# Performance work log

Hardware: AMD Instinct MI355X
Metric: run time of the kernel (lower is better)

Reference implementation:

```python
import jax, jax.numpy as jnp
import numpy as np

N = 50000      # nodes
E = 600000     # edges (avg degree 12)
D = 128        # in_dim == hidden_dim
H = 4          # heads
HD = 32        # per-head dim (hidden_dim // heads)
NEG = 0.2      # GATv2 leaky_relu negative slope (PyG default)
EPS = 1e-5     # LayerNorm eps


def setup_inputs() -> dict:
    key = jax.random.key(0)
    ks = jax.random.split(key, 4)
    inp = {
        "x": jax.random.normal(ks[0], (N, D), jnp.float32),
        "edge_index": jax.random.randint(ks[1], (2, E), 0, N, dtype=jnp.int32),
    }
    glorot = 1.0 / np.sqrt(D)
    for i in range(2):
        k = jax.random.split(jax.random.fold_in(ks[2], i), 8)
        inp[f"Wl{i}"] = jax.random.normal(k[0], (D, H * HD), jnp.float32) * glorot
        inp[f"bl{i}"] = jnp.zeros((H * HD,), jnp.float32)
        inp[f"Wr{i}"] = jax.random.normal(k[1], (D, H * HD), jnp.float32) * glorot
        inp[f"br{i}"] = jnp.zeros((H * HD,), jnp.float32)
        inp[f"att{i}"] = jax.random.normal(k[2], (H, HD), jnp.float32) * (1.0 / np.sqrt(HD))
        inp[f"bias{i}"] = jnp.zeros((H * HD,), jnp.float32)
        inp[f"g{i}"] = jnp.ones((H * HD,), jnp.float32)   # LayerNorm gamma
        inp[f"b{i}"] = jnp.zeros((H * HD,), jnp.float32)  # LayerNorm beta
    return inp


def _gat_layer(h, src, dst, Wl, bl, Wr, br, att, bias, g, b):
    # GATv2: x_l from source nodes, x_r from destination nodes
    xl = (h @ Wl + bl).reshape(N, H, HD)
    xr = (h @ Wr + br).reshape(N, H, HD)
    # edge-wise attention score: att . leaky_relu(x_l[j] + x_r[i])
    e = jax.nn.leaky_relu(xl[src] + xr[dst], NEG)          # [E, H, HD]
    score = jnp.einsum('ehd,hd->eh', e, att)               # [E, H]
    # segment softmax over edges sharing a destination
    m = jax.ops.segment_max(score, dst, num_segments=N)    # [N, H]
    m = jnp.where(jnp.isfinite(m), m, 0.0)                 # isolated nodes
    ex = jnp.exp(score - m[dst])
    den = jax.ops.segment_sum(ex, dst, num_segments=N)
    alpha = ex / (den[dst] + 1e-16)                        # [E, H]
    # scatter-add aggregation of source messages
    out = jax.ops.segment_sum(alpha[:, :, None] * xl[src], dst, num_segments=N)
    out = out.reshape(N, H * HD) + bias
    # LayerNorm + ELU (dropout is identity in eval mode)
    mu = out.mean(-1, keepdims=True)
    var = out.var(-1, keepdims=True)
    out = (out - mu) / jnp.sqrt(var + EPS) * g + b
    return jax.nn.elu(out)


def reference(x, edge_index, Wl0, bl0, Wr0, br0, att0, bias0, g0, b0,
              Wl1, bl1, Wr1, br1, att1, bias1, g1, b1):
    src, dst = edge_index[0], edge_index[1]
    h = _gat_layer(x, src, dst, Wl0, bl0, Wr0, br0, att0, bias0, g0, b0)
    h = _gat_layer(h, src, dst, Wl1, bl1, Wr1, br1, att1, bias1, g1, b1)
    return h
```

## Files before the change

kernel.cpp:

```cpp
#include <hip/hip_runtime.h>

#define NN 50000
#define NN_PAD 50016
#define NE 600000
#define DD 128
#define NH 4
#define RB_CNT 3125
#define RB_PAD 3128
#define COUNT_BLKS ((NE + 255) / 256)
#define ZERO_BLKS ((NN / 4 + 255) / 256)

#define SCAN_T 512
#define SCAN_B ((NN + SCAN_T - 1) / SCAN_T)

#define LOG2E 1.44269504088896340736f

typedef short s16x8 __attribute__((ext_vector_type(8)));
typedef float f32x4 __attribute__((ext_vector_type(4)));

__device__ __forceinline__ unsigned short bfh(float f) {
  unsigned u = __float_as_uint(f);
  return (unsigned short)((u + 0x7fffu + ((u >> 16) & 1u)) >> 16);
}
__device__ __forceinline__ float bff(unsigned short h) {
  return __uint_as_float(((unsigned)h) << 16);
}

template <int CTRL>
__device__ __forceinline__ float dpp_add(float x) {
  int y = __builtin_amdgcn_update_dpp(0, __float_as_int(x), CTRL, 0xf, 0xf, true);
  return x + __int_as_float(y);
}

__device__ __forceinline__ void prep_a_body(
    int tid, const float* __restrict__ h,
    unsigned short* __restrict__ Ah, unsigned short* __restrict__ Am) {
  int lr = tid & 15;
  int g = (tid >> 4) & 3;
  int kt = (tid >> 6) & 3;
  int rb = tid >> 8;
  int row = rb * 16 + lr;
  const float* p = h + (size_t)row * DD + kt * 32 + 4 * g;
  float4 f0 = *(const float4*)(p);
  float4 f1 = *(const float4*)(p + 16);
  float fs[8] = {f0.x, f0.y, f0.z, f0.w, f1.x, f1.y, f1.z, f1.w};
  s16x8 hi, mid;
#pragma unroll
  for (int e = 0; e < 8; e++) {
    unsigned short hh = bfh(fs[e]);
    hi[e] = (short)hh;
    mid[e] = (short)bfh(fs[e] - bff(hh));
  }
  *(s16x8*)(Ah + (size_t)tid * 8) = hi;
  *(s16x8*)(Am + (size_t)tid * 8) = mid;
}

__device__ __forceinline__ void prep_w_body(
    int tid, const float* __restrict__ Wl0, const float* __restrict__ Wr0,
    const float* __restrict__ Wl1, const float* __restrict__ Wr1,
    unsigned short* __restrict__ Bh, unsigned short* __restrict__ Bm) {
  int lay = tid >> 12;
  int t = tid & 4095;
  int lr = t & 15;
  int g = (t >> 4) & 3;
  int kt = (t >> 6) & 3;
  int ct = t >> 8;
  int col = ct * 16 + lr;
  const float* W = (col < DD) ? (lay ? Wl1 : Wl0) : (lay ? Wr1 : Wr0);
  int cc = (col < DD) ? col : col - DD;
  s16x8 hi, mid;
#pragma unroll
  for (int e = 0; e < 8; e++) {
    int k = kt * 32 + ((e >> 2) << 4) + 4 * g + (e & 3);
    float w = W[(size_t)k * DD + cc];
    unsigned short hh = bfh(w);
    hi[e] = (short)hh;
    mid[e] = (short)bfh(w - bff(hh));
  }
  *(s16x8*)(Bh + (size_t)tid * 8) = hi;
  *(s16x8*)(Bm + (size_t)tid * 8) = mid;
}

__device__ __forceinline__ void gemm_body16(
    int bid, int tid,
    const unsigned short* __restrict__ Ah, const unsigned short* __restrict__ Am,
    const unsigned short* __restrict__ Bh, const unsigned short* __restrict__ Bm,
    const float* __restrict__ blv, const float* __restrict__ brv,
    unsigned short* __restrict__ xlb, unsigned short* __restrict__ xrb) {
  const int lane = tid & 63;
  const int wv = tid >> 6;
  const int lr = lane & 15;
  const int g = lane >> 4;

  f32x4 acc[4];
#pragma unroll
  for (int nt = 0; nt < 4; nt++)
#pragma unroll
    for (int e = 0; e < 4; e++) acc[nt][e] = 0.f;

#pragma unroll
  for (int kt = 0; kt < 4; kt++) {
    size_t aoff = ((((size_t)(bid * 4 + kt)) * 4 + g) * 16 + lr) * 8;
    s16x8 ah = *(const s16x8*)(Ah + aoff);
    s16x8 am = *(const s16x8*)(Am + aoff);
    s16x8 bh[4], bm[4];
#pragma unroll
    for (int nt = 0; nt < 4; nt++) {
      int ct = wv * 4 + nt;
      size_t off = ((((size_t)(ct * 4 + kt)) * 4 + g) * 16 + lr) * 8;
      bh[nt] = *(const s16x8*)(Bh + off);
      bm[nt] = *(const s16x8*)(Bm + off);
    }
#pragma unroll
    for (int nt = 0; nt < 4; nt++) {
      acc[nt] = __builtin_amdgcn_mfma_f32_16x16x32_bf16(ah, bh[nt], acc[nt], 0, 0, 0);
      acc[nt] = __builtin_amdgcn_mfma_f32_16x16x32_bf16(ah, bm[nt], acc[nt], 0, 0, 0);
      acc[nt] = __builtin_amdgcn_mfma_f32_16x16x32_bf16(am, bh[nt], acc[nt], 0, 0, 0);
    }
  }

#pragma unroll
  for (int nt = 0; nt < 4; nt++) {
    int col = wv * 64 + nt * 16 + lr;
    unsigned short* dst = (col < DD) ? (xlb + col) : (xrb + (col - DD));
    float bv = (col < DD) ? blv[col] : brv[col - DD];
    int rowb = bid * 16 + 4 * g;
#pragma unroll
    for (int r = 0; r < 4; r++)
      dst[(size_t)(rowb + r) * DD] = bfh(acc[nt][r] + bv);
  }
}

__global__ __launch_bounds__(256) void init_fused(
    const float* __restrict__ h,
    const float* __restrict__ Wl0, const float* __restrict__ Wr0,
    const float* __restrict__ Wl1, const float* __restrict__ Wr1,
    unsigned short* __restrict__ Ah, unsigned short* __restrict__ Am,
    unsigned short* __restrict__ Bh, unsigned short* __restrict__ Bm,
    int* __restrict__ deg, int* __restrict__ colsrc) {
  int b = blockIdx.x;
  if (b < RB_CNT) {
    prep_a_body(b * 256 + threadIdx.x, h, Ah, Am);
  } else if (b < RB_CNT + 32) {
    prep_w_body((b - RB_CNT) * 256 + threadIdx.x, Wl0, Wr0, Wl1, Wr1, Bh, Bm);
  } else {
    int i = ((b - RB_CNT - 32) * 256 + threadIdx.x) << 2;
    if (i < NN) {
      if (i + 3 < NN) *(int4*)(deg + i) = make_int4(0, 0, 0, 0);
      else for (int k = i; k < NN; k++) deg[k] = 0;
    }
    if (b == RB_CNT + 32 && threadIdx.x < 16) colsrc[NE + threadIdx.x] = 0;
  }
}

__global__ __launch_bounds__(256) void count_gemm_fused(
    const unsigned short* __restrict__ Ah, const unsigned short* __restrict__ Am,
    const unsigned short* __restrict__ Bh, const unsigned short* __restrict__ Bm,
    const float* __restrict__ blv, const float* __restrict__ brv,
    unsigned short* __restrict__ xlb, unsigned short* __restrict__ xrb,
    const int* __restrict__ ei, int* __restrict__ deg) {
  int b = blockIdx.x;
  if (b < RB_CNT) {
    gemm_body16(b, threadIdx.x, Ah, Am, Bh, Bm, blv, brv, xlb, xrb);
  } else {
    int e = (b - RB_CNT) * 256 + threadIdx.x;
    if (e < NE) atomicAdd(deg + ei[NE + e], 1);
  }
}

__global__ __launch_bounds__(256) void dual_gemm_mfma(
    const unsigned short* __restrict__ Ah, const unsigned short* __restrict__ Am,
    const unsigned short* __restrict__ Bh, const unsigned short* __restrict__ Bm,
    const float* __restrict__ blv, const float* __restrict__ brv,
    unsigned short* __restrict__ xlb, unsigned short* __restrict__ xrb) {
  gemm_body16(blockIdx.x, threadIdx.x, Ah, Am, Bh, Bm, blv, brv, xlb, xrb);
}

__global__ __launch_bounds__(SCAN_T) void scan_partial(
    const int* __restrict__ deg, int* __restrict__ rowp, int* __restrict__ bsum) {
  __shared__ int buf[SCAN_T];
  int b = blockIdx.x, t = threadIdx.x;
  int i = b * SCAN_T + t;
  int v = (i < NN) ? deg[i] : 0;
  buf[t] = v;
  __syncthreads();
  for (int o = 1; o < SCAN_T; o <<= 1) {
    int add = (t >= o) ? buf[t - o] : 0;
    __syncthreads();
    buf[t] += add;
    __syncthreads();
  }
  if (i < NN) rowp[i] = buf[t] - v;
  if (t == SCAN_T - 1) bsum[b] = buf[t];
}

__global__ __launch_bounds__(SCAN_T) void scan_finish(
    const int* __restrict__ bsum, int* __restrict__ rowp, int* __restrict__ cur) {
  __shared__ int sb[SCAN_T];
  int b = blockIdx.x, t = threadIdx.x;
  int v = (t < SCAN_B) ? bsum[t] : 0;
  sb[t] = v;
  __syncthreads();
  for (int o = 1; o < SCAN_T; o <<= 1) {
    int add = (t >= o) ? sb[t - o] : 0;
    __syncthreads();
    sb[t] += add;
    __syncthreads();
  }
  int boff = sb[b] - bsum[b];
  int i = b * SCAN_T + t;
  if (i < NN) {
    int r = rowp[i] + boff;
    rowp[i] = r;
    cur[i] = r;
  }
  if (b == 0 && t == 0) rowp[NN] = sb[SCAN_B - 1];
}

__global__ void scatter_src(const int* __restrict__ ei,
                            int* __restrict__ cur, int* __restrict__ colsrc) {
  int e = blockIdx.x * 256 + threadIdx.x;
  if (e < NE) {
    int d = ei[NE + e];
    int p = atomicAdd(cur + d, 1);
    colsrc[p] = ei[e] << 8;
  }
}

template <int SPLIT>
__global__ __launch_bounds__(256) void fused_edge_agg(
    const int* __restrict__ rowp, const int* __restrict__ colsrc,
    const unsigned short* __restrict__ xlb, const unsigned short* __restrict__ xrb,
    const float* __restrict__ att, const float* __restrict__ bias,
    const float* __restrict__ gam, const float* __restrict__ bet,
    float* __restrict__ out, unsigned short* __restrict__ Oh,
    unsigned short* __restrict__ Om) {
  int node = (blockIdx.x * 256 + threadIdx.x) >> 5;
  if (node >= NN) return;
  int il = threadIdx.x & 31;
  int d0 = il << 2;

  ushort4 xru = *(const ushort4*)(xrb + (size_t)node * DD + d0);
  float4 xrv; xrv.x = bff(xru.x); xrv.y = bff(xru.y);
  xrv.z = bff(xru.z); xrv.w = bff(xru.w);
  float4 atv = *(const float4*)(att + d0);
  atv.x *= LOG2E; atv.y *= LOG2E; atv.z *= LOG2E; atv.w *= LOG2E;
  int j0 = rowp[node];
  int j1 = rowp[node + 1];

  float den = 0.f;
  float a0 = 0.f, a1 = 0.f, a2 = 0.f, a3 = 0.f;
  const char* xlb8 = (const char*)xlb;
  const int goff = il << 3;

  ushort4 gA0, gA1, gA2, gA3;
  int sB0 = 0, sB1 = 0, sB2 = 0, sB3 = 0;
  if (j0 < j1) {
    int sA0 = colsrc[j0], sA1 = colsrc[j0 + 1];
    int sA2 = colsrc[j0 + 2], sA3 = colsrc[j0 + 3];
    gA0 = *(const ushort4*)(xlb8 + (size_t)(unsigned)(sA0 + goff));
    gA1 = *(const ushort4*)(xlb8 + (size_t)(unsigned)(sA1 + goff));
    gA2 = *(const ushort4*)(xlb8 + (size_t)(unsigned)(sA2 + goff));
    gA3 = *(const ushort4*)(xlb8 + (size_t)(unsigned)(sA3 + goff));
    sB0 = colsrc[j0 + 4]; sB1 = colsrc[j0 + 5];
    sB2 = colsrc[j0 + 6]; sB3 = colsrc[j0 + 7];
  }

  for (int j = j0; j < j1; j += 4) {
    ushort4 gB0 = *(const ushort4*)(xlb8 + (size_t)(unsigned)(sB0 + goff));
    ushort4 gB1 = *(const ushort4*)(xlb8 + (size_t)(unsigned)(sB1 + goff));
    ushort4 gB2 = *(const ushort4*)(xlb8 + (size_t)(unsigned)(sB2 + goff));
    ushort4 gB3 = *(const ushort4*)(xlb8 + (size_t)(unsigned)(sB3 + goff));
    int sC0 = colsrc[j + 8],  sC1 = colsrc[j + 9];
    int sC2 = colsrc[j + 10], sC3 = colsrc[j + 11];

    bool v1 = (j + 1) < j1, v2 = (j + 2) < j1, v3 = (j + 3) < j1;
    float x00 = bff(gA0.x), x01 = bff(gA0.y), x02 = bff(gA0.z), x03 = bff(gA0.w);
    float x10 = bff(gA1.x), x11 = bff(gA1.y), x12 = bff(gA1.z), x13 = bff(gA1.w);
    float x20 = bff(gA2.x), x21 = bff(gA2.y), x22 = bff(gA2.z), x23 = bff(gA2.w);
    float x30 = bff(gA3.x), x31 = bff(gA3.y), x32 = bff(gA3.z), x33 = bff(gA3.w);

    float t0, t1, t2, t3;
    t0 = x00 + xrv.x; t1 = x01 + xrv.y; t2 = x02 + xrv.z; t3 = x03 + xrv.w;
    t0 = fmaxf(t0, 0.2f * t0); t1 = fmaxf(t1, 0.2f * t1);
    t2 = fmaxf(t2, 0.2f * t2); t3 = fmaxf(t3, 0.2f * t3);
    float p0 = (t0 * atv.x + t1 * atv.y) + (t2 * atv.z + t3 * atv.w);
    t0 = x10 + xrv.x; t1 = x11 + xrv.y; t2 = x12 + xrv.z; t3 = x13 + xrv.w;
    t0 = fmaxf(t0, 0.2f * t0); t1 = fmaxf(t1, 0.2f * t1);
    t2 = fmaxf(t2, 0.2f * t2); t3 = fmaxf(t3, 0.2f * t3);
    float p1 = (t0 * atv.x + t1 * atv.y) + (t2 * atv.z + t3 * atv.w);
    t0 = x20 + xrv.x; t1 = x21 + xrv.y; t2 = x22 + xrv.z; t3 = x23 + xrv.w;
    t0 = fmaxf(t0, 0.2f * t0); t1 = fmaxf(t1, 0.2f * t1);
    t2 = fmaxf(t2, 0.2f * t2); t3 = fmaxf(t3, 0.2f * t3);
    float p2 = (t0 * atv.x + t1 * atv.y) + (t2 * atv.z + t3 * atv.w);
    t0 = x30 + xrv.x; t1 = x31 + xrv.y; t2 = x32 + xrv.z; t3 = x33 + xrv.w;
    t0 = fmaxf(t0, 0.2f * t0); t1 = fmaxf(t1, 0.2f * t1);
    t2 = fmaxf(t2, 0.2f * t2); t3 = fmaxf(t3, 0.2f * t3);
    float p3 = (t0 * atv.x + t1 * atv.y) + (t2 * atv.z + t3 * atv.w);

    p0 = dpp_add<0xB1>(p0);  p1 = dpp_add<0xB1>(p1);
    p2 = dpp_add<0xB1>(p2);  p3 = dpp_add<0xB1>(p3);
    p0 = dpp_add<0x4E>(p0);  p1 = dpp_add<0x4E>(p1);
    p2 = dpp_add<0x4E>(p2);  p3 = dpp_add<0x4E>(p3);
    p0 = dpp_add<0x141>(p0); p1 = dpp_add<0x141>(p1);
    p2 = dpp_add<0x141>(p2); p3 = dpp_add<0x141>(p3);

    float w0 = exp2f(p0);
    float w1 = v1 ? exp2f(p1) : 0.f;
    float w2 = v2 ? exp2f(p2) : 0.f;
    float w3 = v3 ? exp2f(p3) : 0.f;
    den += (w0 + w1) + (w2 + w3);
    a0 += (w0 * x00 + w1 * x10) + (w2 * x20 + w3 * x30);
    a1 += (w0 * x01 + w1 * x11) + (w2 * x21 + w3 * x31);
    a2 += (w0 * x02 + w1 * x12) + (w2 * x22 + w3 * x32);
    a3 += (w0 * x03 + w1 * x13) + (w2 * x23 + w3 * x33);

    gA0 = gB0; gA1 = gB1; gA2 = gB2; gA3 = gB3;
    sB0 = sC0; sB1 = sC1; sB2 = sC2; sB3 = sC3;
  }

  float inv = 1.f / (den + 1e-16f);
  float4 bi = *(const float4*)(bias + d0);
  float vx0 = a0 * inv + bi.x, vx1 = a1 * inv + bi.y;
  float vx2 = a2 * inv + bi.z, vx3 = a3 * inv + bi.w;

  float s1f = (vx0 + vx1) + (vx2 + vx3);
  float s2f = (vx0 * vx0 + vx1 * vx1) + (vx2 * vx2 + vx3 * vx3);
  s1f = dpp_add<0xB1>(s1f);  s2f = dpp_add<0xB1>(s2f);
  s1f = dpp_add<0x4E>(s1f);  s2f = dpp_add<0x4E>(s2f);
  s1f = dpp_add<0x124>(s1f); s2f = dpp_add<0x124>(s2f);
  s1f = dpp_add<0x128>(s1f); s2f = dpp_add<0x128>(s2f);
  s1f += __shfl_xor(s1f, 16); s2f += __shfl_xor(s2f, 16);
  float mean = s1f * (1.f / 128.f);
  float var = s2f * (1.f / 128.f) - mean * mean;
  float rstd = rsqrtf(var + 1e-5f);
  float4 gm = *(const float4*)(gam + d0);
  float4 bt = *(const float4*)(bet + d0);
  float n0 = (vx0 - mean) * rstd * gm.x + bt.x;
  float n1 = (vx1 - mean) * rstd * gm.y + bt.y;
  float n2 = (vx2 - mean) * rstd * gm.z + bt.z;
  float n3 = (vx3 - mean) * rstd * gm.w + bt.w;
  n0 = n0 > 0.f ? n0 : __expf(n0) - 1.f;
  n1 = n1 > 0.f ? n1 : __expf(n1) - 1.f;
  n2 = n2 > 0.f ? n2 : __expf(n2) - 1.f;
  n3 = n3 > 0.f ? n3 : __expf(n3) - 1.f;

  if (SPLIT) {
    int rb = node >> 4, lr16 = node & 15;
    int kt = d0 >> 5;
    int g = (d0 & 15) >> 2;
    int e0 = ((d0 >> 4) & 1) << 2;
    size_t off = ((((size_t)(rb * 4 + kt)) * 4 + g) * 16 + lr16) * 8 + e0;
    unsigned short h0 = bfh(n0), h1 = bfh(n1), h2 = bfh(n2), h3 = bfh(n3);
    ushort4 hv; hv.x = h0; hv.y = h1; hv.z = h2; hv.w = h3;
    ushort4 mv;
    mv.x = bfh(n0 - bff(h0)); mv.y = bfh(n1 - bff(h1));
    mv.z = bfh(n2 - bff(h2)); mv.w = bfh(n3 - bff(h3));
    *(ushort4*)(Oh + off) = hv;
    *(ushort4*)(Om + off) = mv;
  } else {
    float4 o; o.x = n0; o.y = n1; o.z = n2; o.w = n3;
    *(float4*)(out + (size_t)node * DD + d0) = o;
  }
}

extern "C" void kernel_launch(void* const* d_in, const int* in_sizes, int n_in,
                              void* d_out, int out_size, void* d_ws, size_t ws_size,
                              hipStream_t stream) {
  const float* x  = (const float*)d_in[0];
  const int*   ei = (const int*)d_in[1];
  const float* Wl[2]   = {(const float*)d_in[2],  (const float*)d_in[10]};
  const float* bl[2]   = {(const float*)d_in[3],  (const float*)d_in[11]};
  const float* Wr[2]   = {(const float*)d_in[4],  (const float*)d_in[12]};
  const float* br[2]   = {(const float*)d_in[5],  (const float*)d_in[13]};
  const float* att[2]  = {(const float*)d_in[6],  (const float*)d_in[14]};
  const float* bias[2] = {(const float*)d_in[7],  (const float*)d_in[15]};
  const float* gam[2]  = {(const float*)d_in[8],  (const float*)d_in[16]};
  const float* bet[2]  = {(const float*)d_in[9],  (const float*)d_in[17]};
  float* out = (float*)d_out;

  char* w = (char*)d_ws;
  auto carve = [&](size_t bytes) {
    char* p = w;
    w += (bytes + 255) & ~(size_t)255;
    return p;
  };
  unsigned short* xlb = (unsigned short*)carve((size_t)NN_PAD * DD * 2);
  unsigned short* xrb = (unsigned short*)carve((size_t)NN_PAD * DD * 2);
  int*   deg    = (int*)carve((size_t)NN * 4);
  int*   cur    = (int*)carve((size_t)NN * 4);
  int*   rowp   = (int*)carve((size_t)(NN + 1) * 4);
  int*   colsrc = (int*)carve((size_t)(NE + 16) * 4);
  int*   bsum   = (int*)carve((size_t)SCAN_B * 4);
  unsigned short* Ah = (unsigned short*)carve((size_t)RB_PAD * 2048 * 2);
  unsigned short* Am = (unsigned short*)carve((size_t)RB_PAD * 2048 * 2);
  unsigned short* Bh = (unsigned short*)carve((size_t)8192 * 8 * 2);
  unsigned short* Bm = (unsigned short*)carve((size_t)8192 * 8 * 2);

  init_fused<<<RB_CNT + 32 + ZERO_BLKS, 256, 0, stream>>>(
      x, Wl[0], Wr[0], Wl[1], Wr[1], Ah, Am, Bh, Bm, deg, colsrc);
  count_gemm_fused<<<RB_CNT + COUNT_BLKS, 256, 0, stream>>>(
      Ah, Am, Bh, Bm, bl[0], br[0], xlb, xrb, ei, deg);
  scan_partial<<<SCAN_B, SCAN_T, 0, stream>>>(deg, rowp, bsum);
  scan_finish<<<SCAN_B, SCAN_T, 0, stream>>>(bsum, rowp, cur);
  scatter_src<<<COUNT_BLKS, 256, 0, stream>>>(ei, cur, colsrc);
  fused_edge_agg<1><<<(NN * 32 + 255) / 256, 256, 0, stream>>>(
      rowp, colsrc, xlb, xrb, att[0], bias[0], gam[0], bet[0], out, Ah, Am);
  dual_gemm_mfma<<<RB_CNT, 256, 0, stream>>>(
      Ah, Am, Bh + (size_t)4096 * 8, Bm + (size_t)4096 * 8,
      bl[1], br[1], xlb, xrb);
  fused_edge_agg<0><<<(NN * 32 + 255) / 256, 256, 0, stream>>>(
      rowp, colsrc, xlb, xrb, att[1], bias[1], gam[1], bet[1], out, Ah, Am);
}
```

Baseline: 186.7 us.

## Make dual GEMM persistent with register-resident weights and split degree count

Replaces the one-tile-per-block GEMM with a kernel where each of 625 blocks handles 5 row tiles and loads the full B fragments (hi and mid) into registers once. This cuts repeated weight loads and block launch overhead. The degree-count atomics now run as their own kernel instead of sharing a launch with the GEMM, which adds a launch and removes the overlap between the two. Keeping 32 s16x8 B fragments per thread raises register pressure and may lower occupancy.

```diff
diff --git a/kernel.cpp b/kernel.cpp
--- a/kernel.cpp
+++ b/kernel.cpp
@@ -7,6 +7,8 @@
 #define NH 4
 #define RB_CNT 3125
 #define RB_PAD 3128
+#define TPB 5
+#define GEMM_GRID 625
 #define COUNT_BLKS ((NE + 255) / 256)
 #define ZERO_BLKS ((NN / 4 + 255) / 256)
 
@@ -79,56 +81,6 @@
   }
   *(s16x8*)(Bh + (size_t)tid * 8) = hi;
   *(s16x8*)(Bm + (size_t)tid * 8) = mid;
-}
-
-__device__ __forceinline__ void gemm_body16(
-    int bid, int tid,
-    const unsigned short* __restrict__ Ah, const unsigned short* __restrict__ Am,
-    const unsigned short* __restrict__ Bh, const unsigned short* __restrict__ Bm,
-    const float* __restrict__ blv, const float* __restrict__ brv,
-    unsigned short* __restrict__ xlb, unsigned short* __restrict__ xrb) {
-  const int lane = tid & 63;
-  const int wv = tid >> 6;
-  const int lr = lane & 15;
-  const int g = lane >> 4;
-
-  f32x4 acc[4];
-#pragma unroll
-  for (int nt = 0; nt < 4; nt++)
-#pragma unroll
-    for (int e = 0; e < 4; e++) acc[nt][e] = 0.f;
-
-#pragma unroll
-  for (int kt = 0; kt < 4; kt++) {
-    size_t aoff = ((((size_t)(bid * 4 + kt)) * 4 + g) * 16 + lr) * 8;
-    s16x8 ah = *(const s16x8*)(Ah + aoff);
-    s16x8 am = *(const s16x8*)(Am + aoff);
-    s16x8 bh[4], bm[4];
-#pragma unroll
-    for (int nt = 0; nt < 4; nt++) {
-      int ct = wv * 4 + nt;
-      size_t off = ((((size_t)(ct * 4 + kt)) * 4 + g) * 16 + lr) * 8;
-      bh[nt] = *(const s16x8*)(Bh + off);
-      bm[nt] = *(const s16x8*)(Bm + off);
-    }
-#pragma unroll
-    for (int nt = 0; nt < 4; nt++) {
-      acc[nt] = __builtin_amdgcn_mfma_f32_16x16x32_bf16(ah, bh[nt], acc[nt], 0, 0, 0);
-      acc[nt] = __builtin_amdgcn_mfma_f32_16x16x32_bf16(ah, bm[nt], acc[nt], 0, 0, 0);
-      acc[nt] = __builtin_amdgcn_mfma_f32_16x16x32_bf16(am, bh[nt], acc[nt], 0, 0, 0);
-    }
-  }
-
-#pragma unroll
-  for (int nt = 0; nt < 4; nt++) {
-    int col = wv * 64 + nt * 16 + lr;
-    unsigned short* dst = (col < DD) ? (xlb + col) : (xrb + (col - DD));
-    float bv = (col < DD) ? blv[col] : brv[col - DD];
-    int rowb = bid * 16 + 4 * g;
-#pragma unroll
-    for (int r = 0; r < 4; r++)
-      dst[(size_t)(rowb + r) * DD] = bfh(acc[nt][r] + bv);
-  }
 }
 
 __global__ __launch_bounds__(256) void init_fused(
@@ -153,27 +105,71 @@
   }
 }
 
-__global__ __launch_bounds__(256) void count_gemm_fused(
-    const unsigned short* __restrict__ Ah, const unsigned short* __restrict__ Am,
-    const unsigned short* __restrict__ Bh, const unsigned short* __restrict__ Bm,
-    const float* __restrict__ blv, const float* __restrict__ brv,
-    unsigned short* __restrict__ xlb, unsigned short* __restrict__ xrb,
-    const int* __restrict__ ei, int* __restrict__ deg) {
-  int b = blockIdx.x;
-  if (b < RB_CNT) {
-    gemm_body16(b, threadIdx.x, Ah, Am, Bh, Bm, blv, brv, xlb, xrb);
-  } else {
-    int e = (b - RB_CNT) * 256 + threadIdx.x;
-    if (e < NE) atomicAdd(deg + ei[NE + e], 1);
-  }
-}
-
-__global__ __launch_bounds__(256) void dual_gemm_mfma(
+__global__ void count_deg(const int* __restrict__ ei, int* __restrict__ deg) {
+  int e = blockIdx.x * 256 + threadIdx.x;
+  if (e < NE) atomicAdd(deg + ei[NE + e], 1);
+}
+
+__global__ __launch_bounds__(256) void gemm_persist(
     const unsigned short* __restrict__ Ah, const unsigned short* __restrict__ Am,
     const unsigned short* __restrict__ Bh, const unsigned short* __restrict__ Bm,
     const float* __restrict__ blv, const float* __restrict__ brv,
     unsigned short* __restrict__ xlb, unsigned short* __restrict__ xrb) {
-  gemm_body16(blockIdx.x, threadIdx.x, Ah, Am, Bh, Bm, blv, brv, xlb, xrb);
+  const int tid = threadIdx.x;
+  const int lane = tid & 63;
+  const int wv = tid >> 6;
+  const int lr = lane & 15;
+  const int g = lane >> 4;
+
+  s16x8 bh[4][4], bm[4][4];
+#pragma unroll
+  for (int kt = 0; kt < 4; kt++)
+#pragma unroll
+    for (int nt = 0; nt < 4; nt++) {
+      int ct = wv * 4 + nt;
+      size_t off = ((((size_t)(ct * 4 + kt)) * 4 + g) * 16 + lr) * 8;
+      bh[kt][nt] = *(const s16x8*)(Bh + off);
+      bm[kt][nt] = *(const s16x8*)(Bm + off);
+    }
+
+  float bv[4];
+  unsigned short* dstb[4];
+#pragma unroll
+  for (int nt = 0; nt < 4; nt++) {
+    int col = wv * 64 + nt * 16 + lr;
+    bv[nt] = (col < DD) ? blv[col] : brv[col - DD];
+    dstb[nt] = (col < DD) ? (xlb + col) : (xrb + (col - DD));
+  }
+
+  for (int t = 0; t < TPB; t++) {
+    int bid = blockIdx.x * TPB + t;
+    s16x8 ah[4], am[4];
+#pragma unroll
+    for (int kt = 0; kt < 4; kt++) {
+      size_t aoff = ((((size_t)(bid * 4 + kt)) * 4 + g) * 16 + lr) * 8;
+      ah[kt] = *(const s16x8*)(Ah + aoff);
+      am[kt] = *(const s16x8*)(Am + aoff);
+    }
+    f32x4 acc[4];
+#pragma unroll
+    for (int nt = 0; nt < 4; nt++)
+#pragma unroll
+      for (int e = 0; e < 4; e++) acc[nt][e] = 0.f;
+#pragma unroll
+    for (int kt = 0; kt < 4; kt++)
+#pragma unroll
+      for (int nt = 0; nt < 4; nt++) {
+        acc[nt] = __builtin_amdgcn_mfma_f32_16x16x32_bf16(ah[kt], bh[kt][nt], acc[nt], 0, 0, 0);
+        acc[nt] = __builtin_amdgcn_mfma_f32_16x16x32_bf16(ah[kt], bm[kt][nt], acc[nt], 0, 0, 0);
+        acc[nt] = __builtin_amdgcn_mfma_f32_16x16x32_bf16(am[kt], bh[kt][nt], acc[nt], 0, 0, 0);
+      }
+    int rowb = bid * 16 + 4 * g;
+#pragma unroll
+    for (int nt = 0; nt < 4; nt++)
+#pragma unroll
+      for (int r = 0; r < 4; r++)
+        dstb[nt][(size_t)(rowb + r) * DD] = bfh(acc[nt][r] + bv[nt]);
+  }
 }
 
 __global__ __launch_bounds__(SCAN_T) void scan_partial(
@@ -399,14 +395,15 @@
 
   init_fused<<<RB_CNT + 32 + ZERO_BLKS, 256, 0, stream>>>(
       x, Wl[0], Wr[0], Wl[1], Wr[1], Ah, Am, Bh, Bm, deg, colsrc);
-  count_gemm_fused<<<RB_CNT + COUNT_BLKS, 256, 0, stream>>>(
-      Ah, Am, Bh, Bm, bl[0], br[0], xlb, xrb, ei, deg);
+  count_deg<<<COUNT_BLKS, 256, 0, stream>>>(ei, deg);
+  gemm_persist<<<GEMM_GRID, 256, 0, stream>>>(
+      Ah, Am, Bh, Bm, bl[0], br[0], xlb, xrb);
   scan_partial<<<SCAN_B, SCAN_T, 0, stream>>>(deg, rowp, bsum);
   scan_finish<<<SCAN_B, SCAN_T, 0, stream>>>(bsum, rowp, cur);
   scatter_src<<<COUNT_BLKS, 256, 0, stream>>>(ei, cur, colsrc);
   fused_edge_agg<1><<<(NN * 32 + 255) / 256, 256, 0, stream>>>(
       rowp, colsrc, xlb, xrb, att[0], bias[0], gam[0], bet[0], out, Ah, Am);
-  dual_gemm_mfma<<<RB_CNT, 256, 0, stream>>>(
+  gemm_persist<<<GEMM_GRID, 256, 0, stream>>>(
       Ah, Am, Bh + (size_t)4096 * 8, Bm + (size_t)4096 * 8,
       bl[1], br[1], xlb, xrb);
   fused_edge_agg<0><<<(NN * 32 + 255) / 256, 256, 0, stream>>>(
```

After: 193.6 us. 1.04x slower.
